# Optimization experiments

Hardware: AMD Instinct MI355X
Metric: run time of the kernel (lower is better)

## Reference

```python
import jax, jax.numpy as jnp
import numpy as np

jax.config.update("jax_enable_x64", True)  # torch lfilter runs in double precision

SR = 24000
RES_SIZE = 64
R_MIN, R_MAX = 0.9999, 0.99999
B, T = 4, 120000


def setup_inputs() -> dict:
    # Probe coefficients (fixed buffers, computed exactly as in Probe.__init__)
    theta_min = 2 * np.pi * 10.0 / SR
    theta_max = 2 * np.pi * 100.0 / SR
    theta = np.exp(np.linspace(np.log(theta_min), np.log(theta_max), RES_SIZE))
    radii = np.linspace(R_MIN, R_MAX, RES_SIZE)
    a1 = -2.0 * radii * np.cos(theta)          # [C]
    a2 = radii ** 2                             # [C]
    b0 = (1.0 - radii) * 0.5                    # [C]

    # Tank mixing weight: orthogonal init, shape [out=64, in=128] (rows orthonormal)
    rng = np.random.default_rng(1337)
    q, _ = np.linalg.qr(rng.standard_normal((2 * RES_SIZE, RES_SIZE)))  # [128,64], orthonormal cols
    W = q.T.astype(np.float32)                  # [64,128]

    key = jax.random.key(0)
    k1, k2 = jax.random.split(key)
    pred = jax.random.normal(k1, (B, 1, T), dtype=jnp.float32)
    target = jax.random.normal(k2, (B, 1, T), dtype=jnp.float32)
    return {
        "pred": pred,
        "target": target,
        "a1": jnp.asarray(a1, jnp.float64),
        "a2": jnp.asarray(a2, jnp.float64),
        "b0": jnp.asarray(b0, jnp.float64),
        "W": jnp.asarray(W, jnp.float32),
    }


def _biquad_bank(x, a1, a2, b0):
    """Biquad filter bank. x: [N, T] float64; coeffs: [C]. Returns [N, C, T].
    y[t] = b0*x[t] - a1*y[t-1] - a2*y[t-2]  (a0 = 1, b1 = b2 = 0, clamp=False)
    """
    n = x.shape[0]
    c = a1.shape[0]

    def step(carry, xt):
        y1, y2 = carry  # each [N, C]
        y = b0[None, :] * xt[:, None] - a1[None, :] * y1 - a2[None, :] * y2
        return (y, y1), y

    init = (jnp.zeros((n, c), x.dtype), jnp.zeros((n, c), x.dtype))
    _, ys = jax.lax.scan(step, init, x.T)      # [T, N, C]
    return jnp.transpose(ys, (1, 2, 0))        # [N, C, T]


def _probe(x, a1, a2, b0):
    """x: [B,1,T] float -> [B, 2C, T] float32 (fwd state ++ bwd state)."""
    xs = x[:, 0, :].astype(jnp.float64)        # [B, T]
    # run forward-time and reversed-time filters in one batched scan
    both = jnp.concatenate([xs, xs[:, ::-1]], axis=0)       # [2B, T]
    ys = _biquad_bank(both, a1, a2, b0)                      # [2B, C, T]
    nb = xs.shape[0]
    fwd_state = ys[:nb]                                      # [B, C, T]
    bwd_state = ys[nb:][:, :, ::-1]                          # [B, C, T] (flipped back)
    return jnp.concatenate([fwd_state, bwd_state], axis=1).astype(jnp.float32)


def _tank(x, W):
    """x: [B, 2C, T], W: [C, 2C] -> tanh(W @ x): [B, C, T]."""
    return jnp.tanh(jnp.einsum("bct,oc->bot", x, W))


def reference(pred, target, a1, a2, b0, W):
    t = pred.shape[-1]
    margin = t // 3
    p_emb = _tank(_probe(pred, a1, a2, b0), W)    # [B, C, T]
    t_emb = _tank(_probe(target, a1, a2, b0), W)  # [B, C, T]
    p_valid = p_emb[..., margin:t - margin]
    t_valid = t_emb[..., margin:t - margin]
    return jnp.mean(jnp.abs(p_valid - t_valid))
```

## Files before the change

### kernel.cpp

```cpp
#include <hip/hip_runtime.h>

#define T_LEN 120000
#define LBLK 160
#define PBLK 750
#define SEG_LEN 25
#define NSEG 30
#define CCH 32
#define NCHUNK (LBLK / CCH)
#define BATCH 4
#define K0 250
#define NKV 250
#define DENOM 20480000.0
#define YSTR 130

typedef _Float16 half8 __attribute__((ext_vector_type(8)));
typedef float f32x4 __attribute__((ext_vector_type(4)));

__device__ __forceinline__ float fast_tanh(float x) {
  float e = __expf(2.0f * x);
  return 1.0f - 2.0f / (e + 1.0f);
}

__device__ __forceinline__ bool coeffs_are_f64(const void* a2p) {
  double probe = *(const double*)a2p;
  return probe > 0.9 && probe < 1.0;
}
__device__ __forceinline__ double coeff_d(const void* p, bool f64, int ch) {
  return f64 ? ((const double*)p)[ch] : (double)((const float*)p)[ch];
}

__device__ __forceinline__ void mat_pow(double A1, double A2, int e,
                                        double& r00, double& r01,
                                        double& r10, double& r11) {
  double m00 = -A1, m01 = -A2, m10 = 1.0, m11 = 0.0;
  r00 = 1.0; r01 = 0.0; r10 = 0.0; r11 = 1.0;
  while (e) {
    if (e & 1) {
      double t00 = r00 * m00 + r01 * m10, t01 = r00 * m01 + r01 * m11;
      double t10 = r10 * m00 + r11 * m10, t11 = r10 * m01 + r11 * m11;
      r00 = t00; r01 = t01; r10 = t10; r11 = t11;
    }
    e >>= 1;
    if (e) {
      double t00 = m00 * m00 + m01 * m10, t01 = m00 * m01 + m01 * m11;
      double t10 = m10 * m00 + m11 * m10, t11 = m10 * m01 + m11 * m11;
      m00 = t00; m01 = t01; m10 = t10; m11 = t11;
    }
  }
}

__global__ __launch_bounds__(64) void pass1(
    const float* __restrict__ pred, const float* __restrict__ tgt,
    const void* a1p, const void* a2p, const void* b0p,
    double* __restrict__ fbuf)
{
  int k = blockIdx.x, r = blockIdx.y;
  int i = r >> 3, d = (r >> 2) & 1, b = r & 3;
  const float* sig = (i ? tgt : pred) + b * T_LEN;
  __shared__ float xs[LBLK];
  int base = k * LBLK;
  for (int j = threadIdx.x; j < LBLK; j += 64)
    xs[j] = d ? sig[T_LEN - 1 - (base + j)] : sig[base + j];
  __syncthreads();
  int ch = threadIdx.x;
  bool f64 = coeffs_are_f64(a2p);
  float A1 = (float)coeff_d(a1p, f64, ch);
  float A2 = (float)coeff_d(a2p, f64, ch);
  float B0 = (float)coeff_d(b0p, f64, ch);
  float y1 = 0.0f, y2 = 0.0f;
  for (int j = 0; j < LBLK; ++j) {
    float y = fmaf(-A1, y1, fmaf(-A2, y2, B0 * xs[j]));
    y2 = y1; y1 = y;
  }
  int s = r * 64 + ch;
  ((double2*)fbuf)[(size_t)k * 1024 + s] = make_double2((double)y1, (double)y2);
}

__global__ __launch_bounds__(64) void pass2a(
    const void* a1p, const void* a2p,
    const double* __restrict__ fbuf, double* __restrict__ sbuf)
{
  int seg = blockIdx.x >> 4;
  int s = ((blockIdx.x & 15) << 6) + threadIdx.x;
  int ch = s & 63;
  bool f64 = coeffs_are_f64(a2p);
  double r00, r01, r10, r11;
  mat_pow(coeff_d(a1p, f64, ch), coeff_d(a2p, f64, ch), LBLK, r00, r01, r10, r11);
  const double2* fb = (const double2*)fbuf;
  double y1 = 0.0, y2 = 0.0;
  for (int jj = 0; jj < SEG_LEN / 5; ++jj) {
    size_t kb = (size_t)(seg * SEG_LEN + jj * 5) * 1024 + s;
    double2 f0 = fb[kb], f1 = fb[kb + 1024], f2 = fb[kb + 2048],
            f3 = fb[kb + 3072], f4 = fb[kb + 4096];
    double n1, n2;
    n1 = r00*y1 + r01*y2 + f0.x; n2 = r10*y1 + r11*y2 + f0.y; y1=n1; y2=n2;
    n1 = r00*y1 + r01*y2 + f1.x; n2 = r10*y1 + r11*y2 + f1.y; y1=n1; y2=n2;
    n1 = r00*y1 + r01*y2 + f2.x; n2 = r10*y1 + r11*y2 + f2.y; y1=n1; y2=n2;
    n1 = r00*y1 + r01*y2 + f3.x; n2 = r10*y1 + r11*y2 + f3.y; y1=n1; y2=n2;
    n1 = r00*y1 + r01*y2 + f4.x; n2 = r10*y1 + r11*y2 + f4.y; y1=n1; y2=n2;
  }
  ((double2*)sbuf)[(size_t)seg * 1024 + s] = make_double2(y1, y2);
}

__global__ __launch_bounds__(256) void pass2b(
    const void* a1p, const void* a2p,
    const double* __restrict__ sbuf, double* __restrict__ tbuf)
{
  int s = blockIdx.x * 256 + threadIdx.x;
  int ch = s & 63;
  bool f64 = coeffs_are_f64(a2p);
  double r00, r01, r10, r11;
  mat_pow(coeff_d(a1p, f64, ch), coeff_d(a2p, f64, ch), LBLK * SEG_LEN,
          r00, r01, r10, r11);
  const double2* sb = (const double2*)sbuf;
  double2* tb = (double2*)tbuf;
  double y1 = 0.0, y2 = 0.0;
  #pragma unroll 1
  for (int half = 0; half < 2; ++half) {
    int base = half * 15;
    double2 f[15];
    #pragma unroll
    for (int q = 0; q < 15; ++q) f[q] = sb[(size_t)(base + q) * 1024 + s];
    #pragma unroll
    for (int q = 0; q < 15; ++q) {
      tb[(size_t)(base + q) * 1024 + s] = make_double2(y1, y2);
      double n1 = r00 * y1 + r01 * y2 + f[q].x;
      double n2 = r10 * y1 + r11 * y2 + f[q].y;
      y1 = n1; y2 = n2;
    }
  }
}

__global__ __launch_bounds__(256, 4) void pass3(
    const float* __restrict__ pred, const float* __restrict__ tgt,
    const void* a1p, const void* a2p, const void* b0p,
    const float* __restrict__ W, const double* __restrict__ fbuf,
    const double* __restrict__ tbuf, double* __restrict__ wsum)
{
  int k = K0 + blockIdx.x;
  int b = blockIdx.y;
  int tid = threadIdx.x;
  __shared__ __align__(16) _Float16 ys[2][64 * YSTR];
  __shared__ float red[4];

  int g = tid >> 6, lane = tid & 63;
  int gu = __builtin_amdgcn_readfirstlane(g);
  int iu = gu >> 1, du = gu & 1;
  int ch = lane;
  int n0 = gu * 16;
  int lm = lane & 15, quad = lane >> 4;

  bool f64 = coeffs_are_f64(a2p);
  double A1d = coeff_d(a1p, f64, ch), A2d = coeff_d(a2p, f64, ch);
  double B0d = coeff_d(b0p, f64, ch);
  float A1 = (float)A1d, A2 = (float)A2d, B0 = (float)B0d;
  float IA2 = (float)(1.0 / A2d);

  int m = du ? (PBLK - k) : k;
  int seg = m / SEG_LEN, j = m - seg * SEG_LEN;
  int s = (iu * 8 + du * 4 + b) * 64 + ch;
  double r00, r01, r10, r11;
  mat_pow(A1d, A2d, LBLK, r00, r01, r10, r11);
  double2 v0 = ((const double2*)tbuf)[(size_t)seg * 1024 + s];
  double y1 = v0.x, y2 = v0.y;
  const double2* fb = (const double2*)fbuf + (size_t)(seg * SEG_LEN) * 1024 + s;
  #pragma unroll 1
  for (int bb = 0; bb < 24; bb += 8) {
    double2 f[8];
    #pragma unroll
    for (int q = 0; q < 8; ++q) f[q] = fb[(size_t)(bb + q) * 1024];
    #pragma unroll
    for (int q = 0; q < 8; ++q) {
      if (bb + q < j) {
        double n1 = r00 * y1 + r01 * y2 + f[q].x;
        double n2 = r10 * y1 + r11 * y2 + f[q].y;
        y1 = n1; y2 = n2;
      }
    }
  }
  float st0 = (float)y1, st1 = (float)y2;

  half8 wf[4][4];
  #pragma unroll
  for (int m0 = 0; m0 < 4; ++m0) {
    #pragma unroll
    for (int k0 = 0; k0 < 4; ++k0) {
      const float* wp = W + (m0 * 16 + lm) * 128 + k0 * 32 + quad * 8;
      float4 wa = *(const float4*)wp, wb = *(const float4*)(wp + 4);
      half8 h;
      h[0] = (_Float16)wa.x; h[1] = (_Float16)wa.y;
      h[2] = (_Float16)wa.z; h[3] = (_Float16)wa.w;
      h[4] = (_Float16)wb.x; h[5] = (_Float16)wb.y;
      h[6] = (_Float16)wb.z; h[7] = (_Float16)wb.w;
      wf[m0][k0] = h;
    }
  }

  const float* xp = (iu ? tgt : pred) + b * T_LEN + k * LBLK;

  float loss = 0.0f;
  for (int cc = 0; cc < NCHUNK; ++cc) {
    _Float16* yb = ys[cc & 1];
    if (du == 0) {
      #pragma unroll
      for (int tt = 0; tt < CCH; ++tt) {
        float x = xp[cc * CCH + tt];
        float y = fmaf(-A1, st0, fmaf(-A2, st1, B0 * x));
        yb[(2 * tt + iu) * YSTR + ch] = (_Float16)y;
        st1 = st0; st0 = y;
      }
    } else {
      #pragma unroll
      for (int tt = 0; tt < CCH; ++tt) {
        float x = xp[cc * CCH + tt];
        yb[(2 * tt + iu) * YSTR + 64 + ch] = (_Float16)st0;
        float ym2 = (fmaf(-A1, st1, B0 * x) - st0) * IA2;
        st0 = st1; st1 = ym2;
      }
    }
    __syncthreads();

    const _Float16* yrow = &yb[(n0 + lm) * YSTR + quad * 8];
    half8 bf0 = *(const half8*)(yrow);
    half8 bf1 = *(const half8*)(yrow + 32);
    half8 bf2 = *(const half8*)(yrow + 64);
    half8 bf3 = *(const half8*)(yrow + 96);
    #pragma unroll
    for (int m0 = 0; m0 < 4; ++m0) {
      f32x4 c = {0.f, 0.f, 0.f, 0.f};
      c = __builtin_amdgcn_mfma_f32_16x16x32_f16(wf[m0][0], bf0, c, 0, 0, 0);
      c = __builtin_amdgcn_mfma_f32_16x16x32_f16(wf[m0][1], bf1, c, 0, 0, 0);
      c = __builtin_amdgcn_mfma_f32_16x16x32_f16(wf[m0][2], bf2, c, 0, 0, 0);
      c = __builtin_amdgcn_mfma_f32_16x16x32_f16(wf[m0][3], bf3, c, 0, 0, 0);
      #pragma unroll
      for (int r = 0; r < 4; ++r) {
        float vv = fast_tanh(c[r]);
        float p = __shfl_xor(vv, 1);
        loss += fabsf(vv - p);
      }
    }
  }

  #pragma unroll
  for (int off = 32; off > 0; off >>= 1) loss += __shfl_down(loss, off);
  if ((tid & 63) == 0) red[tid >> 6] = loss;
  __syncthreads();
  if (tid == 0) atomicAdd(wsum, (double)(red[0] + red[1] + red[2] + red[3]));
}

__global__ void finalize(const double* __restrict__ wsum, float* __restrict__ out) {
  out[0] = (float)(wsum[0] / DENOM);
}

extern "C" void kernel_launch(void* const* d_in, const int* in_sizes, int n_in,
                              void* d_out, int out_size, void* d_ws, size_t ws_size,
                              hipStream_t stream) {
  const float* pred = (const float*)d_in[0];
  const float* tgt  = (const float*)d_in[1];
  const void* a1p = d_in[2];
  const void* a2p = d_in[3];
  const void* b0p = d_in[4];
  const float* W  = (const float*)d_in[5];
  float* out = (float*)d_out;

  double* base = (double*)d_ws;
  double* wsum = base;
  double* fbuf = base + 8;
  double* sbuf = fbuf + (size_t)PBLK * 1024 * 2;
  double* tbuf = sbuf + (size_t)NSEG * 1024 * 2;

  hipMemsetAsync(wsum, 0, sizeof(double), stream);
  pass1<<<dim3(PBLK, 16), 64, 0, stream>>>(pred, tgt, a1p, a2p, b0p, fbuf);
  pass2a<<<NSEG * 16, 64, 0, stream>>>(a1p, a2p, fbuf, sbuf);
  pass2b<<<dim3(4), 256, 0, stream>>>(a1p, a2p, sbuf, tbuf);
  pass3<<<dim3(NKV, BATCH), 256, 0, stream>>>(pred, tgt, a1p, a2p, b0p,
                                              W, fbuf, tbuf, wsum);
  finalize<<<1, 1, 0, stream>>>(wsum, out);
}
```

Before: 128.0 us.

## Shrink scan blocks and add a per-block initial-state pass for the MFMA stage

Block length drops from 160 to 32 samples, giving many more blocks in the local-scan pass, which now packs five blocks per 320-thread workgroup. A new pass2c propagates segment states down to every block in the valid range and writes per-block initial states, so pass3 no longer runs a serial double-precision catch-up. Each pass3 workgroup now handles two 32-sample blocks with a single sync. The memset is replaced by in-kernel zeroing of 128 spread atomic slots, which finalize reduces. The cost is an extra launch, larger fbuf and ibuf workspaces, and longer serial chains in pass2a and pass2b.

```diff
diff --git a/kernel.cpp b/kernel.cpp
--- a/kernel.cpp
+++ b/kernel.cpp
@@ -1,17 +1,18 @@
 #include <hip/hip_runtime.h>
 
 #define T_LEN 120000
-#define LBLK 160
-#define PBLK 750
+#define LBLK 32
+#define PBLK 3750
 #define SEG_LEN 25
-#define NSEG 30
-#define CCH 32
-#define NCHUNK (LBLK / CCH)
+#define NSEG 150
 #define BATCH 4
-#define K0 250
-#define NKV 250
+#define K0 1250
+#define NKV 1250
+#define IB_LO 1250
+#define IB_HI 2500
 #define DENOM 20480000.0
 #define YSTR 130
+#define NSLOT 128
 
 typedef _Float16 half8 __attribute__((ext_vector_type(8)));
 typedef float f32x4 __attribute__((ext_vector_type(4)));
@@ -49,31 +50,42 @@
   }
 }
 
-__global__ __launch_bounds__(64) void pass1(
+__global__ __launch_bounds__(320) void pass1(
     const float* __restrict__ pred, const float* __restrict__ tgt,
     const void* a1p, const void* a2p, const void* b0p,
-    double* __restrict__ fbuf)
-{
-  int k = blockIdx.x, r = blockIdx.y;
+    double* __restrict__ fbuf, double* __restrict__ wsum)
+{
+  int tid = threadIdx.x;
+  int r = blockIdx.y;
+  if (blockIdx.x == 0 && r == 0 && tid < NSLOT) wsum[tid] = 0.0;
+  int w = __builtin_amdgcn_readfirstlane(tid >> 6);
+  int ch = tid & 63;
   int i = r >> 3, d = (r >> 2) & 1, b = r & 3;
+  int k = blockIdx.x * 5 + w;
   const float* sig = (i ? tgt : pred) + b * T_LEN;
-  __shared__ float xs[LBLK];
   int base = k * LBLK;
-  for (int j = threadIdx.x; j < LBLK; j += 64)
-    xs[j] = d ? sig[T_LEN - 1 - (base + j)] : sig[base + j];
-  __syncthreads();
-  int ch = threadIdx.x;
-  bool f64 = coeffs_are_f64(a2p);
-  float A1 = (float)coeff_d(a1p, f64, ch);
-  float A2 = (float)coeff_d(a2p, f64, ch);
-  float B0 = (float)coeff_d(b0p, f64, ch);
+  const float* xp = sig + (d ? (T_LEN - LBLK - base) : base);
+
+  bool f64c = coeffs_are_f64(a2p);
+  float A1 = (float)coeff_d(a1p, f64c, ch);
+  float A2 = (float)coeff_d(a2p, f64c, ch);
+  float B0 = (float)coeff_d(b0p, f64c, ch);
   float y1 = 0.0f, y2 = 0.0f;
-  for (int j = 0; j < LBLK; ++j) {
-    float y = fmaf(-A1, y1, fmaf(-A2, y2, B0 * xs[j]));
-    y2 = y1; y1 = y;
-  }
-  int s = r * 64 + ch;
-  ((double2*)fbuf)[(size_t)k * 1024 + s] = make_double2((double)y1, (double)y2);
+  if (d == 0) {
+    #pragma unroll
+    for (int j = 0; j < LBLK; ++j) {
+      float y = fmaf(-A1, y1, fmaf(-A2, y2, B0 * xp[j]));
+      y2 = y1; y1 = y;
+    }
+  } else {
+    #pragma unroll
+    for (int j = 0; j < LBLK; ++j) {
+      float y = fmaf(-A1, y1, fmaf(-A2, y2, B0 * xp[LBLK - 1 - j]));
+      y2 = y1; y1 = y;
+    }
+  }
+  ((double2*)fbuf)[(size_t)k * 1024 + r * 64 + ch] =
+      make_double2((double)y1, (double)y2);
 }
 
 __global__ __launch_bounds__(64) void pass2a(
@@ -88,6 +100,7 @@
   mat_pow(coeff_d(a1p, f64, ch), coeff_d(a2p, f64, ch), LBLK, r00, r01, r10, r11);
   const double2* fb = (const double2*)fbuf;
   double y1 = 0.0, y2 = 0.0;
+  #pragma unroll 1
   for (int jj = 0; jj < SEG_LEN / 5; ++jj) {
     size_t kb = (size_t)(seg * SEG_LEN + jj * 5) * 1024 + s;
     double2 f0 = fb[kb], f1 = fb[kb + 1024], f2 = fb[kb + 2048],
@@ -116,14 +129,13 @@
   double2* tb = (double2*)tbuf;
   double y1 = 0.0, y2 = 0.0;
   #pragma unroll 1
-  for (int half = 0; half < 2; ++half) {
-    int base = half * 15;
+  for (int bb = 0; bb < NSEG; bb += 15) {
     double2 f[15];
     #pragma unroll
-    for (int q = 0; q < 15; ++q) f[q] = sb[(size_t)(base + q) * 1024 + s];
+    for (int q = 0; q < 15; ++q) f[q] = sb[(size_t)(bb + q) * 1024 + s];
     #pragma unroll
     for (int q = 0; q < 15; ++q) {
-      tb[(size_t)(base + q) * 1024 + s] = make_double2(y1, y2);
+      tb[(size_t)(bb + q) * 1024 + s] = make_double2(y1, y2);
       double n1 = r00 * y1 + r01 * y2 + f[q].x;
       double n2 = r10 * y1 + r11 * y2 + f[q].y;
       y1 = n1; y2 = n2;
@@ -131,13 +143,46 @@
   }
 }
 
+__global__ __launch_bounds__(64) void pass2c(
+    const void* a1p, const void* a2p,
+    const double* __restrict__ fbuf, const double* __restrict__ tbuf,
+    double* __restrict__ ibuf)
+{
+  int seg = 50 + (blockIdx.x >> 4);
+  int s = ((blockIdx.x & 15) << 6) + threadIdx.x;
+  int ch = s & 63;
+  bool f64 = coeffs_are_f64(a2p);
+  double r00, r01, r10, r11;
+  mat_pow(coeff_d(a1p, f64, ch), coeff_d(a2p, f64, ch), LBLK, r00, r01, r10, r11);
+  const double2* fb = (const double2*)fbuf;
+  double2* ib = (double2*)ibuf;
+  double2 v = ((const double2*)tbuf)[(size_t)seg * 1024 + s];
+  double y1 = v.x, y2 = v.y;
+  #pragma unroll 1
+  for (int jj = 0; jj < SEG_LEN / 5; ++jj) {
+    double2 f[5];
+    #pragma unroll
+    for (int q = 0; q < 5; ++q)
+      f[q] = fb[(size_t)(seg * SEG_LEN + jj * 5 + q) * 1024 + s];
+    #pragma unroll
+    for (int q = 0; q < 5; ++q) {
+      int m = seg * SEG_LEN + jj * 5 + q;
+      if (m <= IB_HI)
+        ib[(size_t)(m - IB_LO) * 1024 + s] = make_double2(y1, y2);
+      double n1 = r00 * y1 + r01 * y2 + f[q].x;
+      double n2 = r10 * y1 + r11 * y2 + f[q].y;
+      y1 = n1; y2 = n2;
+    }
+  }
+}
+
 __global__ __launch_bounds__(256, 4) void pass3(
     const float* __restrict__ pred, const float* __restrict__ tgt,
     const void* a1p, const void* a2p, const void* b0p,
-    const float* __restrict__ W, const double* __restrict__ fbuf,
-    const double* __restrict__ tbuf, double* __restrict__ wsum)
-{
-  int k = K0 + blockIdx.x;
+    const float* __restrict__ W, const double* __restrict__ ibuf,
+    double* __restrict__ wsum)
+{
+  int k0 = K0 + blockIdx.x * 2;
   int b = blockIdx.y;
   int tid = threadIdx.x;
   __shared__ __align__(16) _Float16 ys[2][64 * YSTR];
@@ -156,71 +201,63 @@
   float A1 = (float)A1d, A2 = (float)A2d, B0 = (float)B0d;
   float IA2 = (float)(1.0 / A2d);
 
-  int m = du ? (PBLK - k) : k;
-  int seg = m / SEG_LEN, j = m - seg * SEG_LEN;
-  int s = (iu * 8 + du * 4 + b) * 64 + ch;
-  double r00, r01, r10, r11;
-  mat_pow(A1d, A2d, LBLK, r00, r01, r10, r11);
-  double2 v0 = ((const double2*)tbuf)[(size_t)seg * 1024 + s];
-  double y1 = v0.x, y2 = v0.y;
-  const double2* fb = (const double2*)fbuf + (size_t)(seg * SEG_LEN) * 1024 + s;
-  #pragma unroll 1
-  for (int bb = 0; bb < 24; bb += 8) {
-    double2 f[8];
-    #pragma unroll
-    for (int q = 0; q < 8; ++q) f[q] = fb[(size_t)(bb + q) * 1024];
-    #pragma unroll
-    for (int q = 0; q < 8; ++q) {
-      if (bb + q < j) {
-        double n1 = r00 * y1 + r01 * y2 + f[q].x;
-        double n2 = r10 * y1 + r11 * y2 + f[q].y;
-        y1 = n1; y2 = n2;
-      }
-    }
-  }
-  float st0 = (float)y1, st1 = (float)y2;
-
   half8 wf[4][4];
   #pragma unroll
   for (int m0 = 0; m0 < 4; ++m0) {
     #pragma unroll
-    for (int k0 = 0; k0 < 4; ++k0) {
-      const float* wp = W + (m0 * 16 + lm) * 128 + k0 * 32 + quad * 8;
+    for (int q = 0; q < 4; ++q) {
+      const float* wp = W + (m0 * 16 + lm) * 128 + q * 32 + quad * 8;
       float4 wa = *(const float4*)wp, wb = *(const float4*)(wp + 4);
       half8 h;
       h[0] = (_Float16)wa.x; h[1] = (_Float16)wa.y;
       h[2] = (_Float16)wa.z; h[3] = (_Float16)wa.w;
       h[4] = (_Float16)wb.x; h[5] = (_Float16)wb.y;
       h[6] = (_Float16)wb.z; h[7] = (_Float16)wb.w;
-      wf[m0][k0] = h;
-    }
-  }
-
-  const float* xp = (iu ? tgt : pred) + b * T_LEN + k * LBLK;
+      wf[m0][q] = h;
+    }
+  }
+
+  const float* xp = (iu ? tgt : pred) + b * T_LEN + k0 * LBLK;
+  int s = (iu * 8 + du * 4 + b) * 64 + ch;
+  const double2* ib = (const double2*)ibuf;
+  double2 va, vb;
+  if (du == 0) {
+    va = ib[(size_t)(k0 - IB_LO) * 1024 + s];
+    vb = ib[(size_t)(k0 + 1 - IB_LO) * 1024 + s];
+  } else {
+    va = ib[(size_t)(PBLK - k0 - IB_LO) * 1024 + s];
+    vb = ib[(size_t)(PBLK - k0 - 1 - IB_LO) * 1024 + s];
+  }
+  float sa0 = (float)va.x, sa1 = (float)va.y;
+  float sb0 = (float)vb.x, sb1 = (float)vb.y;
+
+  if (du == 0) {
+    #pragma unroll
+    for (int tt = 0; tt < LBLK; ++tt) {
+      float xa = xp[tt], xb = xp[LBLK + tt];
+      float ya = fmaf(-A1, sa0, fmaf(-A2, sa1, B0 * xa));
+      float yb = fmaf(-A1, sb0, fmaf(-A2, sb1, B0 * xb));
+      ys[0][(2 * tt + iu) * YSTR + ch] = (_Float16)ya;
+      ys[1][(2 * tt + iu) * YSTR + ch] = (_Float16)yb;
+      sa1 = sa0; sa0 = ya; sb1 = sb0; sb0 = yb;
+    }
+  } else {
+    #pragma unroll
+    for (int tt = 0; tt < LBLK; ++tt) {
+      float xa = xp[tt], xb = xp[LBLK + tt];
+      ys[0][(2 * tt + iu) * YSTR + 64 + ch] = (_Float16)sa0;
+      ys[1][(2 * tt + iu) * YSTR + 64 + ch] = (_Float16)sb0;
+      float ra = (fmaf(-A1, sa1, B0 * xa) - sa0) * IA2;
+      float rb = (fmaf(-A1, sb1, B0 * xb) - sb0) * IA2;
+      sa0 = sa1; sa1 = ra; sb0 = sb1; sb1 = rb;
+    }
+  }
+  __syncthreads();
 
   float loss = 0.0f;
-  for (int cc = 0; cc < NCHUNK; ++cc) {
-    _Float16* yb = ys[cc & 1];
-    if (du == 0) {
-      #pragma unroll
-      for (int tt = 0; tt < CCH; ++tt) {
-        float x = xp[cc * CCH + tt];
-        float y = fmaf(-A1, st0, fmaf(-A2, st1, B0 * x));
-        yb[(2 * tt + iu) * YSTR + ch] = (_Float16)y;
-        st1 = st0; st0 = y;
-      }
-    } else {
-      #pragma unroll
-      for (int tt = 0; tt < CCH; ++tt) {
-        float x = xp[cc * CCH + tt];
-        yb[(2 * tt + iu) * YSTR + 64 + ch] = (_Float16)st0;
-        float ym2 = (fmaf(-A1, st1, B0 * x) - st0) * IA2;
-        st0 = st1; st1 = ym2;
-      }
-    }
-    __syncthreads();
-
-    const _Float16* yrow = &yb[(n0 + lm) * YSTR + quad * 8];
+  #pragma unroll
+  for (int kk = 0; kk < 2; ++kk) {
+    const _Float16* yrow = &ys[kk][(n0 + lm) * YSTR + quad * 8];
     half8 bf0 = *(const half8*)(yrow);
     half8 bf1 = *(const half8*)(yrow + 32);
     half8 bf2 = *(const half8*)(yrow + 64);
@@ -245,11 +282,22 @@
   for (int off = 32; off > 0; off >>= 1) loss += __shfl_down(loss, off);
   if ((tid & 63) == 0) red[tid >> 6] = loss;
   __syncthreads();
-  if (tid == 0) atomicAdd(wsum, (double)(red[0] + red[1] + red[2] + red[3]));
-}
-
-__global__ void finalize(const double* __restrict__ wsum, float* __restrict__ out) {
-  out[0] = (float)(wsum[0] / DENOM);
+  if (tid == 0) {
+    int slot = (blockIdx.x * 4 + blockIdx.y) & (NSLOT - 1);
+    atomicAdd(&wsum[slot], (double)(red[0] + red[1] + red[2] + red[3]));
+  }
+}
+
+__global__ __launch_bounds__(128) void finalize(
+    const double* __restrict__ wsum, float* __restrict__ out) {
+  __shared__ double part[2];
+  int tid = threadIdx.x;
+  double v = wsum[tid];
+  #pragma unroll
+  for (int off = 32; off > 0; off >>= 1) v += __shfl_down(v, off);
+  if ((tid & 63) == 0) part[tid >> 6] = v;
+  __syncthreads();
+  if (tid == 0) out[0] = (float)((part[0] + part[1]) / DENOM);
 }
 
 extern "C" void kernel_launch(void* const* d_in, const int* in_sizes, int n_in,
@@ -265,15 +313,16 @@
 
   double* base = (double*)d_ws;
   double* wsum = base;
-  double* fbuf = base + 8;
+  double* fbuf = base + NSLOT;
   double* sbuf = fbuf + (size_t)PBLK * 1024 * 2;
   double* tbuf = sbuf + (size_t)NSEG * 1024 * 2;
-
-  hipMemsetAsync(wsum, 0, sizeof(double), stream);
-  pass1<<<dim3(PBLK, 16), 64, 0, stream>>>(pred, tgt, a1p, a2p, b0p, fbuf);
+  double* ibuf = tbuf + (size_t)NSEG * 1024 * 2;
+
+  pass1<<<dim3(750, 16), 320, 0, stream>>>(pred, tgt, a1p, a2p, b0p, fbuf, wsum);
   pass2a<<<NSEG * 16, 64, 0, stream>>>(a1p, a2p, fbuf, sbuf);
   pass2b<<<dim3(4), 256, 0, stream>>>(a1p, a2p, sbuf, tbuf);
-  pass3<<<dim3(NKV, BATCH), 256, 0, stream>>>(pred, tgt, a1p, a2p, b0p,
-                                              W, fbuf, tbuf, wsum);
-  finalize<<<1, 1, 0, stream>>>(wsum, out);
-}
+  pass2c<<<51 * 16, 64, 0, stream>>>(a1p, a2p, fbuf, tbuf, ibuf);
+  pass3<<<dim3(NKV / 2, BATCH), 256, 0, stream>>>(pred, tgt, a1p, a2p, b0p,
+                                                  W, ibuf, wsum);
+  finalize<<<1, 128, 0, stream>>>(wsum, out);
+}
```

New measurement: 181.2 us. 41.5% more time.

## Precompute 64-sample boundary states and split embedding pass into finer blocks

Applied to the files above, without the earlier changes.

Adds a pass2c kernel that runs the double-precision recurrence over each 160-sample block in the valid window and writes filter state at every 64-sample boundary into a new buffer. pass3 then launches 625x4 blocks that each process only 64 samples from these precomputed states, with no per-block prefix recurrence and no chunk loop. The final atomic reduction is spread across 128 slots, which a wider finalize kernel then sums. The aim is more parallelism and shorter serial chains in pass3, at the cost of an extra kernel launch and a serial 160-step double-precision loop per thread in pass2c.

```diff
diff --git a/kernel.cpp b/kernel.cpp
--- a/kernel.cpp
+++ b/kernel.cpp
@@ -5,13 +5,13 @@
 #define PBLK 750
 #define SEG_LEN 25
 #define NSEG 30
-#define CCH 32
-#define NCHUNK (LBLK / CCH)
 #define BATCH 4
-#define K0 250
-#define NKV 250
+#define JB_LO 625
+#define JB_HI 1250
+#define NJV 625
 #define DENOM 20480000.0
 #define YSTR 130
+#define NSLOT 128
 
 typedef _Float16 half8 __attribute__((ext_vector_type(8)));
 typedef float f32x4 __attribute__((ext_vector_type(4)));
@@ -88,6 +88,7 @@
   mat_pow(coeff_d(a1p, f64, ch), coeff_d(a2p, f64, ch), LBLK, r00, r01, r10, r11);
   const double2* fb = (const double2*)fbuf;
   double y1 = 0.0, y2 = 0.0;
+  #pragma unroll 1
   for (int jj = 0; jj < SEG_LEN / 5; ++jj) {
     size_t kb = (size_t)(seg * SEG_LEN + jj * 5) * 1024 + s;
     double2 f0 = fb[kb], f1 = fb[kb + 1024], f2 = fb[kb + 2048],
@@ -116,14 +117,13 @@
   double2* tb = (double2*)tbuf;
   double y1 = 0.0, y2 = 0.0;
   #pragma unroll 1
-  for (int half = 0; half < 2; ++half) {
-    int base = half * 15;
+  for (int bb = 0; bb < NSEG; bb += 15) {
     double2 f[15];
     #pragma unroll
-    for (int q = 0; q < 15; ++q) f[q] = sb[(size_t)(base + q) * 1024 + s];
+    for (int q = 0; q < 15; ++q) f[q] = sb[(size_t)(bb + q) * 1024 + s];
     #pragma unroll
     for (int q = 0; q < 15; ++q) {
-      tb[(size_t)(base + q) * 1024 + s] = make_double2(y1, y2);
+      tb[(size_t)(bb + q) * 1024 + s] = make_double2(y1, y2);
       double n1 = r00 * y1 + r01 * y2 + f[q].x;
       double n2 = r10 * y1 + r11 * y2 + f[q].y;
       y1 = n1; y2 = n2;
@@ -131,36 +131,24 @@
   }
 }
 
-__global__ __launch_bounds__(256, 4) void pass3(
+__global__ __launch_bounds__(64) void pass2c(
     const float* __restrict__ pred, const float* __restrict__ tgt,
     const void* a1p, const void* a2p, const void* b0p,
-    const float* __restrict__ W, const double* __restrict__ fbuf,
-    const double* __restrict__ tbuf, double* __restrict__ wsum)
-{
-  int k = K0 + blockIdx.x;
-  int b = blockIdx.y;
-  int tid = threadIdx.x;
-  __shared__ __align__(16) _Float16 ys[2][64 * YSTR];
-  __shared__ float red[4];
-
-  int g = tid >> 6, lane = tid & 63;
-  int gu = __builtin_amdgcn_readfirstlane(g);
-  int iu = gu >> 1, du = gu & 1;
-  int ch = lane;
-  int n0 = gu * 16;
-  int lm = lane & 15, quad = lane >> 4;
-
-  bool f64 = coeffs_are_f64(a2p);
-  double A1d = coeff_d(a1p, f64, ch), A2d = coeff_d(a2p, f64, ch);
-  double B0d = coeff_d(b0p, f64, ch);
-  float A1 = (float)A1d, A2 = (float)A2d, B0 = (float)B0d;
-  float IA2 = (float)(1.0 / A2d);
-
-  int m = du ? (PBLK - k) : k;
-  int seg = m / SEG_LEN, j = m - seg * SEG_LEN;
-  int s = (iu * 8 + du * 4 + b) * 64 + ch;
+    const double* __restrict__ fbuf, const double* __restrict__ tbuf,
+    float2* __restrict__ jbuf)
+{
+  int k = 250 + blockIdx.x;
+  int r = blockIdx.y;
+  int ch = threadIdx.x;
+  int i = r >> 3, d = (r >> 2) & 1, b = r & 3;
+  int s = r * 64 + ch;
+  bool f64 = coeffs_are_f64(a2p);
+  double A1 = coeff_d(a1p, f64, ch), A2 = coeff_d(a2p, f64, ch);
+  double B0 = coeff_d(b0p, f64, ch);
   double r00, r01, r10, r11;
-  mat_pow(A1d, A2d, LBLK, r00, r01, r10, r11);
+  mat_pow(A1, A2, LBLK, r00, r01, r10, r11);
+
+  int seg = k / SEG_LEN, j0 = k - seg * SEG_LEN;
   double2 v0 = ((const double2*)tbuf)[(size_t)seg * 1024 + s];
   double y1 = v0.x, y2 = v0.y;
   const double2* fb = (const double2*)fbuf + (size_t)(seg * SEG_LEN) * 1024 + s;
@@ -171,56 +159,100 @@
     for (int q = 0; q < 8; ++q) f[q] = fb[(size_t)(bb + q) * 1024];
     #pragma unroll
     for (int q = 0; q < 8; ++q) {
-      if (bb + q < j) {
+      if (bb + q < j0) {
         double n1 = r00 * y1 + r01 * y2 + f[q].x;
         double n2 = r10 * y1 + r11 * y2 + f[q].y;
         y1 = n1; y2 = n2;
       }
     }
   }
-  float st0 = (float)y1, st1 = (float)y2;
+
+  const float* sig = (i ? tgt : pred) + b * T_LEN;
+  int p0 = k * LBLK;
+  #pragma unroll 1
+  for (int idx = 0; idx < LBLK; ++idx) {
+    int p = p0 + idx;
+    if ((p & 63) == 0) {
+      int m = p >> 6;
+      if (m <= JB_HI)
+        jbuf[(size_t)(m - JB_LO) * 1024 + s] = make_float2((float)y1, (float)y2);
+    }
+    double x = (double)(d ? sig[T_LEN - 1 - p] : sig[p]);
+    double y = fma(-A1, y1, fma(-A2, y2, B0 * x));
+    y2 = y1; y1 = y;
+  }
+}
+
+__global__ __launch_bounds__(256, 4) void pass3(
+    const float* __restrict__ pred, const float* __restrict__ tgt,
+    const void* a1p, const void* a2p, const void* b0p,
+    const float* __restrict__ W, const float2* __restrict__ jbuf,
+    double* __restrict__ wsum)
+{
+  int j = JB_LO + blockIdx.x;
+  int b = blockIdx.y;
+  int tid = threadIdx.x;
+  __shared__ __align__(16) _Float16 ys[128 * YSTR];
+  __shared__ float red[4];
+
+  int g = tid >> 6, lane = tid & 63;
+  int gu = __builtin_amdgcn_readfirstlane(g);
+  int iu = gu >> 1, du = gu & 1;
+  int ch = lane;
+  int lm = lane & 15, quad = lane >> 4;
+
+  bool f64 = coeffs_are_f64(a2p);
+  double A2d = coeff_d(a2p, f64, ch);
+  float A1 = (float)coeff_d(a1p, f64, ch);
+  float A2 = (float)A2d;
+  float B0 = (float)coeff_d(b0p, f64, ch);
+  float IA2 = (float)(1.0 / A2d);
 
   half8 wf[4][4];
   #pragma unroll
   for (int m0 = 0; m0 < 4; ++m0) {
     #pragma unroll
-    for (int k0 = 0; k0 < 4; ++k0) {
-      const float* wp = W + (m0 * 16 + lm) * 128 + k0 * 32 + quad * 8;
+    for (int q = 0; q < 4; ++q) {
+      const float* wp = W + (m0 * 16 + lm) * 128 + q * 32 + quad * 8;
       float4 wa = *(const float4*)wp, wb = *(const float4*)(wp + 4);
       half8 h;
       h[0] = (_Float16)wa.x; h[1] = (_Float16)wa.y;
       h[2] = (_Float16)wa.z; h[3] = (_Float16)wa.w;
       h[4] = (_Float16)wb.x; h[5] = (_Float16)wb.y;
       h[6] = (_Float16)wb.z; h[7] = (_Float16)wb.w;
-      wf[m0][k0] = h;
-    }
-  }
-
-  const float* xp = (iu ? tgt : pred) + b * T_LEN + k * LBLK;
+      wf[m0][q] = h;
+    }
+  }
+
+  int s = (iu * 8 + du * 4 + b) * 64 + ch;
+  int jj = du ? (JB_HI - JB_LO - (j - JB_LO)) : (j - JB_LO);
+  float2 v = jbuf[(size_t)jj * 1024 + s];
+  float st0 = v.x, st1 = v.y;
+
+  const float* xp = (iu ? tgt : pred) + b * T_LEN + j * 64;
+
+  if (du == 0) {
+    #pragma unroll
+    for (int tt = 0; tt < 64; ++tt) {
+      float y = fmaf(-A1, st0, fmaf(-A2, st1, B0 * xp[tt]));
+      ys[(2 * tt + iu) * YSTR + ch] = (_Float16)y;
+      st1 = st0; st0 = y;
+    }
+  } else {
+    #pragma unroll
+    for (int tt = 0; tt < 64; ++tt) {
+      ys[(2 * tt + iu) * YSTR + 64 + ch] = (_Float16)st0;
+      float ym2 = (fmaf(-A1, st1, B0 * xp[tt]) - st0) * IA2;
+      st0 = st1; st1 = ym2;
+    }
+  }
+  __syncthreads();
 
   float loss = 0.0f;
-  for (int cc = 0; cc < NCHUNK; ++cc) {
-    _Float16* yb = ys[cc & 1];
-    if (du == 0) {
-      #pragma unroll
-      for (int tt = 0; tt < CCH; ++tt) {
-        float x = xp[cc * CCH + tt];
-        float y = fmaf(-A1, st0, fmaf(-A2, st1, B0 * x));
-        yb[(2 * tt + iu) * YSTR + ch] = (_Float16)y;
-        st1 = st0; st0 = y;
-      }
-    } else {
-      #pragma unroll
-      for (int tt = 0; tt < CCH; ++tt) {
-        float x = xp[cc * CCH + tt];
-        yb[(2 * tt + iu) * YSTR + 64 + ch] = (_Float16)st0;
-        float ym2 = (fmaf(-A1, st1, B0 * x) - st0) * IA2;
-        st0 = st1; st1 = ym2;
-      }
-    }
-    __syncthreads();
-
-    const _Float16* yrow = &yb[(n0 + lm) * YSTR + quad * 8];
+  #pragma unroll
+  for (int sl = 0; sl < 2; ++sl) {
+    int n0 = sl * 64 + gu * 16;
+    const _Float16* yrow = &ys[(n0 + lm) * YSTR + quad * 8];
     half8 bf0 = *(const half8*)(yrow);
     half8 bf1 = *(const half8*)(yrow + 32);
     half8 bf2 = *(const half8*)(yrow + 64);
@@ -245,11 +277,22 @@
   for (int off = 32; off > 0; off >>= 1) loss += __shfl_down(loss, off);
   if ((tid & 63) == 0) red[tid >> 6] = loss;
   __syncthreads();
-  if (tid == 0) atomicAdd(wsum, (double)(red[0] + red[1] + red[2] + red[3]));
-}
-
-__global__ void finalize(const double* __restrict__ wsum, float* __restrict__ out) {
-  out[0] = (float)(wsum[0] / DENOM);
+  if (tid == 0) {
+    int slot = (blockIdx.x * 4 + blockIdx.y) & (NSLOT - 1);
+    atomicAdd(&wsum[slot], (double)(red[0] + red[1] + red[2] + red[3]));
+  }
+}
+
+__global__ __launch_bounds__(128) void finalize(
+    const double* __restrict__ wsum, float* __restrict__ out) {
+  __shared__ double part[2];
+  int tid = threadIdx.x;
+  double v = wsum[tid];
+  #pragma unroll
+  for (int off = 32; off > 0; off >>= 1) v += __shfl_down(v, off);
+  if ((tid & 63) == 0) part[tid >> 6] = v;
+  __syncthreads();
+  if (tid == 0) out[0] = (float)((part[0] + part[1]) / DENOM);
 }
 
 extern "C" void kernel_launch(void* const* d_in, const int* in_sizes, int n_in,
@@ -265,15 +308,18 @@
 
   double* base = (double*)d_ws;
   double* wsum = base;
-  double* fbuf = base + 8;
+  double* fbuf = base + NSLOT;
   double* sbuf = fbuf + (size_t)PBLK * 1024 * 2;
   double* tbuf = sbuf + (size_t)NSEG * 1024 * 2;
-
-  hipMemsetAsync(wsum, 0, sizeof(double), stream);
+  float2* jbuf = (float2*)(tbuf + (size_t)NSEG * 1024 * 2);
+
+  hipMemsetAsync(wsum, 0, NSLOT * sizeof(double), stream);
   pass1<<<dim3(PBLK, 16), 64, 0, stream>>>(pred, tgt, a1p, a2p, b0p, fbuf);
   pass2a<<<NSEG * 16, 64, 0, stream>>>(a1p, a2p, fbuf, sbuf);
   pass2b<<<dim3(4), 256, 0, stream>>>(a1p, a2p, sbuf, tbuf);
-  pass3<<<dim3(NKV, BATCH), 256, 0, stream>>>(pred, tgt, a1p, a2p, b0p,
-                                              W, fbuf, tbuf, wsum);
-  finalize<<<1, 1, 0, stream>>>(wsum, out);
-}
+  pass2c<<<dim3(251, 16), 64, 0, stream>>>(pred, tgt, a1p, a2p, b0p,
+                                           fbuf, tbuf, jbuf);
+  pass3<<<dim3(NJV, BATCH), 256, 0, stream>>>(pred, tgt, a1p, a2p, b0p,
+                                              W, jbuf, wsum);
+  finalize<<<1, 128, 0, stream>>>(wsum, out);
+}
```

Result: slower. 173.4 us (+35.5%).
